# Optimization experiments

Hardware: AMD Instinct MI355X
Metric: run time of the kernel (lower is better)

The kernel has to match this reference:

```python
import jax, jax.numpy as jnp
import numpy as np

LOG0 = -1e30


def _joint_logp(enc, pred, W_enc, W_pred, b_joint, W_out, b_out):
    # enc [B,T,De], pred [B,U+1,Dp] -> log-probs over full joint lattice [B,T,U+1,V]
    ep = jnp.einsum('btd,dj->btj', enc, W_enc)          # [B,T,J]
    pp = jnp.einsum('bud,dj->buj', pred, W_pred)        # [B,U+1,J]
    h = jnp.tanh(ep[:, :, None, :] + pp[:, None, :, :] + b_joint)  # [B,T,U+1,J]
    logits = jnp.einsum('btuj,jv->btuv', h, W_out) + b_out          # [B,T,U+1,V]
    return jax.nn.log_softmax(logits, axis=-1)


def _rnnt_loss(enc, pred, W_enc, W_pred, b_joint, W_out, b_out,
               labels, enc_lens, label_lens, blank_id):
    B, T, _ = enc.shape
    Up1 = pred.shape[1]
    U = Up1 - 1
    logp = _joint_logp(enc, pred, W_enc, W_pred, b_joint, W_out, b_out)
    blank_lp = logp[..., blank_id]                       # [B,T,U+1]
    # label_lp[b,t,u] = logp[b,t,u,labels[b,u]]
    label_lp = jnp.take_along_axis(
        logp[:, :, :U, :], labels[:, None, :, None], axis=3)[..., 0]  # [B,T,U]

    # alpha recurrence over t; the inner u-recurrence
    #   a[u] = logaddexp(alpha[u]+blank_lp[u], a[u-1]+label_lp[u-1])
    # is a log-space linear recurrence solved in parallel via cumlogsumexp:
    #   with L[u] = sum_{j<u} label_lp[j],  a = L + cumlogsumexp(c - L),  c = alpha + blank_lp
    def step(alpha, t):
        blp = blank_lp[:, t]                              # [B,U+1]
        llp = label_lp[:, t]                              # [B,U]
        c = alpha + blp
        L = jnp.concatenate(
            [jnp.zeros((B, 1), dtype=alpha.dtype), jnp.cumsum(llp, axis=1)], axis=1)
        a_new = L + jax.lax.cumlogsumexp(c - L, axis=1)
        alpha = jnp.where((t < enc_lens)[:, None], a_new, alpha)
        return alpha, None

    alpha0 = jnp.full((B, Up1), LOG0, dtype=enc.dtype).at[:, 0].set(0.0)
    alpha, _ = jax.lax.scan(step, alpha0, jnp.arange(T))

    bidx = jnp.arange(B)
    terminal_blank = blank_lp[bidx, enc_lens - 1, label_lens]   # [B]
    alpha_U = alpha[bidx, label_lens]                           # [B]
    return jnp.mean(-(alpha_U + terminal_blank))


def setup_inputs() -> dict:
    key = jax.random.key(0)
    ks = jax.random.split(key, 9)
    B, T, U = 8, 256, 64
    De, Dp, J, V = 640, 640, 512, 1024
    enc = jax.random.normal(ks[0], (B, T, De), dtype=jnp.float32)
    pred = jax.random.normal(ks[1], (B, U + 1, Dp), dtype=jnp.float32)
    labels = jax.random.randint(ks[2], (B, U), 1, V).astype(jnp.int32)
    enc_lens = jax.random.randint(ks[3], (B,), T // 2, T + 1).astype(jnp.int32)
    label_lens = jax.random.randint(ks[4], (B,), U // 2, U + 1).astype(jnp.int32)
    W_enc = jax.random.normal(ks[5], (De, J), dtype=jnp.float32) * (De ** -0.5)
    W_pred = jax.random.normal(ks[6], (Dp, J), dtype=jnp.float32) * (Dp ** -0.5)
    b_joint = jnp.zeros((J,), dtype=jnp.float32)
    W_out = jax.random.normal(ks[7], (J, V), dtype=jnp.float32) * (J ** -0.5)
    b_out = jnp.zeros((V,), dtype=jnp.float32)
    return {"enc": enc, "pred": pred, "W_enc": W_enc, "W_pred": W_pred,
            "b_joint": b_joint, "W_out": W_out, "b_out": b_out,
            "labels": labels, "enc_lens": enc_lens, "label_lens": label_lens,
            "blank_id": 0}


def reference(enc, pred, W_enc, W_pred, b_joint, W_out, b_out,
              labels, enc_lens, label_lens, blank_id):
    return _rnnt_loss(enc, pred, W_enc, W_pred, b_joint, W_out, b_out,
                      labels, enc_lens, label_lens, blank_id)
```

## Files before the change

kernel.cpp:

```cpp
#include <hip/hip_runtime.h>
#include <math.h>

#define B_   8
#define T_   256
#define U_   64
#define UP1  65
#define DE   640
#define J_   512
#define V_   1024
#define NCELL (B_ * T_ * UP1)
#define LOG0 -1e30f
#define NSEG 8
#define SEGLEN 32
#define MLD  66

typedef __attribute__((ext_vector_type(4))) float f32x4;

template<int CTRL, int RM>
__device__ __forceinline__ float dppz(float x) {
    return __builtin_bit_cast(float,
        __builtin_amdgcn_update_dpp(0, __builtin_bit_cast(int, x), CTRL, RM, 0xf, false));
}
template<int CTRL, int RM>
__device__ __forceinline__ float dpps(float x) {
    int xi = __builtin_bit_cast(int, x);
    return __builtin_bit_cast(float,
        __builtin_amdgcn_update_dpp(xi, xi, CTRL, RM, 0xf, false));
}
__device__ __forceinline__ float wave_prefix_sum(float v) {
    v += dppz<0x111, 0xf>(v);
    v += dppz<0x112, 0xf>(v);
    v += dppz<0x114, 0xf>(v);
    v += dppz<0x118, 0xf>(v);
    v += dppz<0x142, 0xa>(v);
    v += dppz<0x143, 0xc>(v);
    return v;
}
__device__ __forceinline__ float wave_max_all(float v) {
    v = fmaxf(v, dpps<0x111, 0xf>(v));
    v = fmaxf(v, dpps<0x112, 0xf>(v));
    v = fmaxf(v, dpps<0x114, 0xf>(v));
    v = fmaxf(v, dpps<0x118, 0xf>(v));
    v = fmaxf(v, dpps<0x142, 0xa>(v));
    v = fmaxf(v, dpps<0x143, 0xc>(v));
    return __builtin_bit_cast(float,
        __builtin_amdgcn_readlane(__builtin_bit_cast(int, v), 63));
}
__device__ __forceinline__ float rdlane(float v, int l) {
    return __builtin_bit_cast(float,
        __builtin_amdgcn_readlane(__builtin_bit_cast(int, v), l));
}

__device__ __forceinline__ unsigned hb8(unsigned m, unsigned cb) {
    return m * 512u + (cb ^ ((m & 15u) << 3));
}

__global__ __launch_bounds__(256) void gemm_in(const float* __restrict__ A,
                                               const float* __restrict__ W,
                                               const float* __restrict__ bias,
                                               float* __restrict__ C, int M) {
    __shared__ float As[16][32];
    __shared__ float Bs[16][64];
    int tid  = threadIdx.x;
    int row0 = blockIdx.x * 32;
    int col0 = blockIdx.y * 64;
    int tx = tid & 15, ty = tid >> 4;
    float acc[2][4] = {};
    int ar  = tid >> 3;
    int ak2 = (tid & 7) * 2;
    int bkr = tid >> 4;
    int bcq = tid & 15;
    for (int k0 = 0; k0 < DE; k0 += 16) {
        float2 av = make_float2(0.f, 0.f);
        int arow = row0 + ar;
        if (arow < M) av = *(const float2*)&A[arow * DE + k0 + ak2];
        As[ak2][ar]     = av.x;
        As[ak2 + 1][ar] = av.y;
        *(float4*)&Bs[bkr][bcq * 4] = *(const float4*)&W[(k0 + bkr) * J_ + col0 + bcq * 4];
        __syncthreads();
#pragma unroll
        for (int k = 0; k < 16; ++k) {
            float a0 = As[k][ty * 2], a1 = As[k][ty * 2 + 1];
            float4 b4 = *(const float4*)&Bs[k][tx * 4];
            float b[4] = {b4.x, b4.y, b4.z, b4.w};
#pragma unroll
            for (int j = 0; j < 4; ++j) {
                acc[0][j] += a0 * b[j];
                acc[1][j] += a1 * b[j];
            }
        }
        __syncthreads();
    }
#pragma unroll
    for (int i = 0; i < 2; ++i) {
        int row = row0 + ty * 2 + i;
        if (row >= M) continue;
#pragma unroll
        for (int j = 0; j < 4; ++j) {
            int col = col0 + tx * 4 + j;
            float v = acc[i][j];
            if (bias) v += bias[col];
            C[row * J_ + col] = v;
        }
    }
}

__global__ __launch_bounds__(256) void wt_kernel(const float* __restrict__ W,
                                                 unsigned char* __restrict__ Wf) {
    __shared__ float tile[32][33];
    int tid = threadIdx.x;
    int tx = tid & 31, ty = tid >> 5;
    int v0 = blockIdx.x * 32, k0 = blockIdx.y * 32;
#pragma unroll
    for (int i = 0; i < 4; ++i)
        tile[ty + i * 8][tx] = W[(size_t)(k0 + ty + i * 8) * V_ + v0 + tx];
    __syncthreads();
    if (tid < 128) {
        int vl = tid >> 2, lg = tid & 3;
        int v  = v0 + vl;
        float x[8];
#pragma unroll
        for (int j = 0; j < 8; ++j) x[j] = tile[lg * 8 + j][vl];
        int lo = 0, hi = 0;
        lo = __builtin_amdgcn_cvt_pk_fp8_f32(x[0], x[1], lo, false);
        lo = __builtin_amdgcn_cvt_pk_fp8_f32(x[2], x[3], lo, true);
        hi = __builtin_amdgcn_cvt_pk_fp8_f32(x[4], x[5], hi, false);
        hi = __builtin_amdgcn_cvt_pk_fp8_f32(x[6], x[7], hi, true);
        int tl = v >> 4, ln = v & 15, kt = k0 >> 5;
        *(int2*)(Wf + tl * 8192 + kt * 512 + (lg * 16 + ln) * 8) = make_int2(lo, hi);
    }
}

__global__ __launch_bounds__(512) void hgen_kernel(const float* __restrict__ ep,
                                                   const float* __restrict__ pp,
                                                   unsigned char* __restrict__ hG) {
    int tid  = threadIdx.x;
    int tile = blockIdx.x;
    unsigned char* outb = hG + (size_t)tile * 32768;
#pragma unroll
    for (int i = 0; i < 4; ++i) {
        int g   = tid + i * 512;
        int row = g >> 5;
        int lin9 = (g & 31) * 16;
        unsigned swz = ((unsigned)(row & 15)) << 3;
        int k0   = lin9 ^ (int)(swz & ~8u);
        int swap = row & 1;
        int cell = tile * 64 + row;
        unsigned epRow = (unsigned)cell / 65u;
        int u = cell - (int)epRow * 65;
        int b = (int)(epRow >> 8);
        const float* epr = ep + (size_t)epRow * J_ + k0;
        const float* ppr = pp + (size_t)(b * UP1 + u) * J_ + k0;
        float t[16];
#pragma unroll
        for (int q = 0; q < 4; ++q) {
            float4 e = *(const float4*)(epr + q * 4);
            float4 p = *(const float4*)(ppr + q * 4);
            float xs[4] = {e.x + p.x, e.y + p.y, e.z + p.z, e.w + p.w};
#pragma unroll
            for (int j = 0; j < 4; ++j) {
                float e2 = __expf(2.f * xs[j]);
                t[q * 4 + j] = 1.f - 2.f / (e2 + 1.f);
            }
        }
        int a0 = 0, a1 = 0, b0 = 0, b1 = 0;
        a0 = __builtin_amdgcn_cvt_pk_fp8_f32(t[0], t[1], a0, false);
        a0 = __builtin_amdgcn_cvt_pk_fp8_f32(t[2], t[3], a0, true);
        a1 = __builtin_amdgcn_cvt_pk_fp8_f32(t[4], t[5], a1, false);
        a1 = __builtin_amdgcn_cvt_pk_fp8_f32(t[6], t[7], a1, true);
        b0 = __builtin_amdgcn_cvt_pk_fp8_f32(t[8], t[9], b0, false);
        b0 = __builtin_amdgcn_cvt_pk_fp8_f32(t[10], t[11], b0, true);
        b1 = __builtin_amdgcn_cvt_pk_fp8_f32(t[12], t[13], b1, false);
        b1 = __builtin_amdgcn_cvt_pk_fp8_f32(t[14], t[15], b1, true);
        int4 w = swap ? make_int4(b0, b1, a0, a1) : make_int4(a0, a1, b0, b1);
        *(int4*)(outb + g * 16) = w;
    }
}

__global__ __launch_bounds__(256, 3) void joint_mfma(const unsigned char* __restrict__ hG,
                                                     const unsigned char* __restrict__ Wf,
                                                     const float* __restrict__ bout,
                                                     const int* __restrict__ labels,
                                                     const int* __restrict__ pblank,
                                                     float* __restrict__ Spart,
                                                     float* __restrict__ blp,
                                                     float* __restrict__ llp) {
    __shared__ __align__(16) unsigned char hB[64 * 512];
    __shared__ float ps[4][64];

    int tid  = threadIdx.x;
    int bx   = blockIdx.x;
    int tile = (bx >> 5) * 8 + (bx & 7);
    int bh   = (bx >> 3) & 3;
    int c0   = tile * 64;
    int wc = tid >> 6, lane = tid & 63;
    int lg = lane >> 4, ln = lane & 15;

    const long* wfbL = (const long*)Wf + (((bh << 4) + (wc << 2)) << 10) + lane;

    long bf[3][4];
    long af[2][4];

    {
        int4 v[8];
        const int4* g = (const int4*)(hG + (size_t)tile * 32768) + tid;
#pragma unroll
        for (int i = 0; i < 8; ++i) v[i] = g[i * 256];
#pragma unroll
        for (int ni = 0; ni < 4; ++ni) bf[0][ni] = wfbL[ni * 1024];
#pragma unroll
        for (int ni = 0; ni < 4; ++ni) bf[1][ni] = wfbL[ni * 1024 + 64];
#pragma unroll
        for (int i = 0; i < 8; ++i) ((int4*)hB)[tid + i * 256] = v[i];
    }
    __syncthreads();

    f32x4 acc[4][4] = {};
#pragma unroll
    for (int mi = 0; mi < 4; ++mi)
        af[0][mi] = *(const long*)(hB + hb8((unsigned)(mi * 16 + ln), (unsigned)(lg * 8)));

#pragma unroll
    for (int kt = 0; kt < 16; ++kt) {
        const int cur3 = kt % 3;
        const int pf3  = (kt + 2) % 3;
        const int cur  = kt & 1, nxt = cur ^ 1;
#pragma unroll
        for (int ni = 0; ni < 4; ++ni) {
            if (kt < 14) bf[pf3][ni] = wfbL[ni * 1024 + (kt + 2) * 64];
            __builtin_amdgcn_s_setprio(1);
#pragma unroll
            for (int mi = 0; mi < 4; ++mi)
                acc[mi][ni] = __builtin_amdgcn_mfma_f32_16x16x32_fp8_fp8(
                    af[cur][mi], bf[cur3][ni], acc[mi][ni], 0, 0, 0);
            __builtin_amdgcn_s_setprio(0);
            if (ni == 1 && kt < 15) {
#pragma unroll
                for (int mi = 0; mi < 4; ++mi) {
                    unsigned m  = (unsigned)(mi * 16 + ln);
                    unsigned cb = (unsigned)((kt + 1) * 32 + lg * 8);
                    af[nxt][mi] = *(const long*)(hB + hb8(m, cb));
                }
            }
        }
    }

    float bo[4];
#pragma unroll
    for (int ni = 0; ni < 4; ++ni) bo[ni] = bout[(bh << 8) + (wc << 6) + (ni << 4) + ln];
#pragma unroll
    for (int mi = 0; mi < 4; ++mi)
#pragma unroll
        for (int ni = 0; ni < 4; ++ni)
#pragma unroll
            for (int r = 0; r < 4; ++r) acc[mi][ni][r] += bo[ni];

#pragma unroll
    for (int mi = 0; mi < 4; ++mi) {
#pragma unroll
        for (int r = 0; r < 4; ++r) {
            float s = 0.f;
#pragma unroll
            for (int ni = 0; ni < 4; ++ni) s += __expf(acc[mi][ni][r]);
            s += __shfl_xor(s, 1);
            s += __shfl_xor(s, 2);
            s += __shfl_xor(s, 4);
            s += __shfl_xor(s, 8);
            if (ln == 0) ps[wc][mi * 16 + lg * 4 + r] = s;
        }
    }
    __syncthreads();
    if (tid < 64) {
        float S = ps[0][tid] + ps[1][tid] + ps[2][tid] + ps[3][tid];
        Spart[(size_t)bh * NCELL + c0 + tid] = S;
    }

    int blank = *pblank;
#pragma unroll
    for (int mi = 0; mi < 4; ++mi) {
#pragma unroll
        for (int r = 0; r < 4; ++r) {
            int row  = mi * 16 + lg * 4 + r;
            int cell = c0 + row;
            unsigned epRow = (unsigned)cell / 65u;
            int u = cell - (int)epRow * 65;
            int b = (int)(epRow >> 8);
            int lab = (u < U_) ? labels[(b << 6) + u] : -1;
#pragma unroll
            for (int ni = 0; ni < 4; ++ni) {
                int col = (bh << 8) + (wc << 6) + (ni << 4) + ln;
                float lgt = acc[mi][ni][r];
                if (col == blank) blp[cell] = lgt;
                if (col == lab)   llp[(size_t)(((int)epRow << 6) + u)] = lgt;
            }
        }
    }
}

__global__ __launch_bounds__(256) void pass2_kernel(const float* __restrict__ Spart,
                                                    float* __restrict__ blp,
                                                    float* __restrict__ llp) {
    int idx = blockIdx.x * 256 + threadIdx.x;
    if (idx >= NCELL) return;
    float lse = __logf(Spart[idx] + Spart[NCELL + idx] +
                       Spart[2 * NCELL + idx] + Spart[3 * NCELL + idx]);
    blp[idx] -= lse;
    unsigned epRow = (unsigned)idx / 65u;
    int u = idx - (int)epRow * 65;
    if (u < U_) llp[(size_t)((epRow << 6) + u)] -= lse;
}

__global__ __launch_bounds__(64) void segscan_kernel(const float* __restrict__ blp,
                                                     const float* __restrict__ llp,
                                                     const int* __restrict__ enc_lens,
                                                     float* __restrict__ Mbuf) {
    const float K2 = 1.4426950408889634f;
    int idx  = blockIdx.x;
    int v    = idx % 65;
    int seg  = (idx / 65) % NSEG;
    int b    = idx / (65 * NSEG);
    int lane = threadIdx.x;
    int el   = enc_lens[b];
    int t0   = seg * SEGLEN;
    if (t0 >= el) return;
    const float* bb = blp + (size_t)b * T_ * UP1;
    const float* lb = llp + (size_t)b * T_ * U_;

    float bvK[SEGLEN], lvK[SEGLEN], b64K[SEGLEN];
#pragma unroll
    for (int j = 0; j < SEGLEN; ++j) {
        int t  = t0 + j;
        int tc = (t < el) ? t : (el - 1);
        bvK[j]  = bb[tc * UP1 + lane] * K2;
        b64K[j] = bb[tc * UP1 + 64] * K2;
        lvK[j]  = lb[tc * U_ + lane] * K2;
    }

    float alpha   = (lane == v) ? 0.f : LOG0;
    float alpha64 = (v == 64) ? 0.f : LOG0;

#pragma unroll
    for (int j = 0; j < SEGLEN; ++j) {
        if (t0 + j < el) {
            float P = wave_prefix_sum(lvK[j]);
            float L = dpps<0x111, 0xf>(P);
            float P15 = rdlane(P, 15), P31 = rdlane(P, 31), P47 = rdlane(P, 47);
            if (lane == 0)  L = 0.f;
            if (lane == 16) L = P15;
            if (lane == 32) L = P31;
            if (lane == 48) L = P47;
            float P63 = rdlane(P, 63);
            float x   = alpha + bvK[j] - L;
            float x64 = alpha64 + b64K[j] - P63;
            float M = fmaxf(wave_max_all(x), x64);
            float S = wave_prefix_sum(__builtin_amdgcn_exp2f(x - M));
            float S63 = rdlane(S, 63);
            alpha   = L + M + __builtin_amdgcn_logf(S);
            alpha64 = P63 + M +
                      __builtin_amdgcn_logf(S63 + __builtin_amdgcn_exp2f(x64 - M));
        }
    }

    float* col = Mbuf + ((size_t)((b * NSEG + seg) * 65 + v)) * MLD;
    col[lane] = fmaxf(alpha, LOG0);
    if (lane == 0) col[64] = fmaxf(alpha64, LOG0);
}

__global__ __launch_bounds__(64) void apply_kernel(const float* __restrict__ Mbuf,
                                                   const float* __restrict__ blp,
                                                   const int* __restrict__ enc_lens,
                                                   const int* __restrict__ label_lens,
                                                   float* __restrict__ lossBuf) {
    __shared__ float Ml[65 * MLD];
    __shared__ float xv[66];
    const float K2  = 1.4426950408889634f;
    const float LN2 = 0.6931471805599453f;
    int b    = blockIdx.x;
    int lane = threadIdx.x;
    int el = enc_lens[b];
    int ll = label_lens[b];

    xv[lane] = (lane == 0) ? 0.f : LOG0;
    if (lane == 0) xv[64] = LOG0;
    __syncthreads();

    for (int seg = 0; seg < NSEG; ++seg) {
        if (seg * SEGLEN >= el) break;
        const float* src = Mbuf + (size_t)((b * NSEG + seg) * 65) * MLD;
        for (int i = lane; i < 65 * MLD; i += 64) Ml[i] = src[i];
        __syncthreads();
        float m = LOG0;
#pragma unroll 5
        for (int vv = 0; vv < 65; ++vv) m = fmaxf(m, Ml[vv * MLD + lane] + xv[vv]);
        m = fmaxf(m, LOG0);
        float s = 0.f;
#pragma unroll 5
        for (int vv = 0; vv < 65; ++vv)
            s += __builtin_amdgcn_exp2f(Ml[vv * MLD + lane] + xv[vv] - m);
        float y = fmaxf(m + __builtin_amdgcn_logf(s), LOG0);
        float t64  = xv[lane] + Ml[lane * MLD + 64];
        float t64b = xv[64] + Ml[64 * MLD + 64];
        float m64 = fmaxf(fmaxf(wave_max_all(t64), t64b), LOG0);
        float s64 = rdlane(wave_prefix_sum(__builtin_amdgcn_exp2f(t64 - m64)), 63);
        s64 += __builtin_amdgcn_exp2f(t64b - m64);
        float y64 = fmaxf(m64 + __builtin_amdgcn_logf(s64), LOG0);
        __syncthreads();
        xv[lane] = y;
        if (lane == 0) xv[64] = y64;
        __syncthreads();
    }

    if (lane == 0) {
        float aU = (ll < 64) ? xv[ll] : xv[64];
        float term = blp[(size_t)b * T_ * UP1 + (el - 1) * UP1 + ll] * K2;
        lossBuf[b] = -(aU + term) * LN2;
    }
}

__global__ __launch_bounds__(64) void finalize_kernel(const float* __restrict__ lossBuf,
                                                      float* __restrict__ out) {
    if (threadIdx.x == 0) {
        float s = 0.f;
        for (int i = 0; i < B_; ++i) s += lossBuf[i];
        out[0] = s / (float)B_;
    }
}

extern "C" void kernel_launch(void* const* d_in, const int* in_sizes, int n_in,
                              void* d_out, int out_size, void* d_ws, size_t ws_size,
                              hipStream_t stream) {
    (void)in_sizes; (void)n_in; (void)out_size; (void)ws_size;
    const float* enc        = (const float*)d_in[0];
    const float* pred       = (const float*)d_in[1];
    const float* W_enc      = (const float*)d_in[2];
    const float* W_pred     = (const float*)d_in[3];
    const float* b_joint    = (const float*)d_in[4];
    const float* W_out      = (const float*)d_in[5];
    const float* b_out      = (const float*)d_in[6];
    const int*   labels     = (const int*)d_in[7];
    const int*   enc_lens   = (const int*)d_in[8];
    const int*   label_lens = (const int*)d_in[9];
    const int*   blank_id   = (const int*)d_in[10];

    float* ep  = (float*)d_ws;
    float* pp  = ep  + (size_t)B_ * T_ * J_;
    float* blp = pp  + (size_t)B_ * UP1 * J_;
    float* llp = blp + (size_t)B_ * T_ * UP1;
    unsigned char* Wf = (unsigned char*)(llp + (size_t)B_ * T_ * U_);
    float* Spart = (float*)(Wf + (size_t)V_ * J_);
    unsigned char* hG = (unsigned char*)(Spart + (size_t)4 * NCELL);
    float* lossBuf = (float*)(hG + (size_t)NCELL * 512);
    float* Mbuf    = lossBuf + 64;

    wt_kernel<<<dim3(V_ / 32, J_ / 32), dim3(256), 0, stream>>>(W_out, Wf);
    gemm_in<<<dim3((B_ * T_ + 31) / 32, J_ / 64), dim3(256), 0, stream>>>(
        enc, W_enc, b_joint, ep, B_ * T_);
    gemm_in<<<dim3((B_ * UP1 + 31) / 32, J_ / 64), dim3(256), 0, stream>>>(
        pred, W_pred, nullptr, pp, B_ * UP1);
    hgen_kernel<<<dim3(NCELL / 64), dim3(512), 0, stream>>>(ep, pp, hG);
    joint_mfma<<<dim3(NCELL / 64 * 4), dim3(256), 0, stream>>>(
        hG, Wf, b_out, labels, blank_id, Spart, blp, llp);
    pass2_kernel<<<dim3((NCELL + 255) / 256), dim3(256), 0, stream>>>(Spart, blp, llp);
    segscan_kernel<<<dim3(B_ * NSEG * 65), dim3(64), 0, stream>>>(blp, llp, enc_lens,
                                                                  Mbuf);
    apply_kernel<<<dim3(B_), dim3(64), 0, stream>>>(Mbuf, blp, enc_lens, label_lens,
                                                    lossBuf);
    finalize_kernel<<<dim3(1), dim3(64), 0, stream>>>(lossBuf, (float*)d_out);
}
```

Measured before the change: 314.3 us.

## Replace FP32 input projection GEMMs with bf16 MFMA GEMM and prep kernel

Replaces the two scalar FP32 shared-memory GEMMs for the encoder and predictor projections with a prep kernel and a single MFMA GEMM. The prep kernel converts enc, pred and the weights to bf16, pre-swizzling the weights into MFMA fragment layout. The GEMM uses one 64-thread wave per 64x64 tile and prefetches operands through registers. This targets the FP32 VALU cost of the projections. It adds a conversion launch and lowers the projection inputs to bf16 precision. It also reuses the hG buffer as scratch before hgen overwrites it.

```diff
diff --git a/kernel.cpp b/kernel.cpp
--- a/kernel.cpp
+++ b/kernel.cpp
@@ -15,6 +15,13 @@
 #define MLD  66
 
 typedef __attribute__((ext_vector_type(4))) float f32x4;
+typedef __attribute__((ext_vector_type(8))) short short8;
+
+__device__ __forceinline__ unsigned short f2bf(float x) {
+    union { float f; unsigned int u; } c; c.f = x;
+    unsigned int r = (c.u + 0x7fffu + ((c.u >> 16) & 1u)) >> 16;
+    return (unsigned short)r;
+}
 
 template<int CTRL, int RM>
 __device__ __forceinline__ float dppz(float x) {
@@ -55,52 +62,126 @@
     return m * 512u + (cb ^ ((m & 15u) << 3));
 }
 
-__global__ __launch_bounds__(256) void gemm_in(const float* __restrict__ A,
-                                               const float* __restrict__ W,
-                                               const float* __restrict__ bias,
-                                               float* __restrict__ C, int M) {
-    __shared__ float As[16][32];
-    __shared__ float Bs[16][64];
-    int tid  = threadIdx.x;
-    int row0 = blockIdx.x * 32;
-    int col0 = blockIdx.y * 64;
-    int tx = tid & 15, ty = tid >> 4;
-    float acc[2][4] = {};
-    int ar  = tid >> 3;
-    int ak2 = (tid & 7) * 2;
-    int bkr = tid >> 4;
-    int bcq = tid & 15;
-    for (int k0 = 0; k0 < DE; k0 += 16) {
-        float2 av = make_float2(0.f, 0.f);
-        int arow = row0 + ar;
-        if (arow < M) av = *(const float2*)&A[arow * DE + k0 + ak2];
-        As[ak2][ar]     = av.x;
-        As[ak2 + 1][ar] = av.y;
-        *(float4*)&Bs[bkr][bcq * 4] = *(const float4*)&W[(k0 + bkr) * J_ + col0 + bcq * 4];
-        __syncthreads();
-#pragma unroll
-        for (int k = 0; k < 16; ++k) {
-            float a0 = As[k][ty * 2], a1 = As[k][ty * 2 + 1];
-            float4 b4 = *(const float4*)&Bs[k][tx * 4];
-            float b[4] = {b4.x, b4.y, b4.z, b4.w};
-#pragma unroll
-            for (int j = 0; j < 4; ++j) {
-                acc[0][j] += a0 * b[j];
-                acc[1][j] += a1 * b[j];
+__global__ __launch_bounds__(256) void prep_kernel(const float* __restrict__ We,
+                                                   const float* __restrict__ Wp,
+                                                   const float* __restrict__ enc,
+                                                   const float* __restrict__ pred,
+                                                   unsigned short* __restrict__ wf2e,
+                                                   unsigned short* __restrict__ wf2p,
+                                                   unsigned short* __restrict__ encB,
+                                                   unsigned short* __restrict__ predB) {
+    int bx = blockIdx.x, tid = threadIdx.x;
+    if (bx < 320) {
+        const float* W = (bx < 160) ? We : Wp;
+        unsigned short* dst = (bx < 160) ? wf2e : wf2p;
+        int gid = ((bx < 160) ? bx : bx - 160) * 256 + tid;
+        int lane = gid & 63, ktl = gid >> 6;
+        int kt = ktl % 20, tl = ktl / 20;
+        int lg = lane >> 4, ln = lane & 15;
+        int col = tl * 16 + ln;
+        short8 v;
+#pragma unroll
+        for (int j = 0; j < 8; ++j)
+            v[j] = (short)f2bf(W[(size_t)(kt * 32 + lg * 8 + j) * J_ + col]);
+        *(short8*)(dst + (size_t)gid * 8) = v;
+    } else if (bx < 960) {
+        int gid = (bx - 320) * 256 + tid;
+        const float* s = enc + (size_t)gid * 8;
+        float4 a = *(const float4*)s, b = *(const float4*)(s + 4);
+        short8 v;
+        v[0] = (short)f2bf(a.x); v[1] = (short)f2bf(a.y);
+        v[2] = (short)f2bf(a.z); v[3] = (short)f2bf(a.w);
+        v[4] = (short)f2bf(b.x); v[5] = (short)f2bf(b.y);
+        v[6] = (short)f2bf(b.z); v[7] = (short)f2bf(b.w);
+        *(short8*)(encB + (size_t)gid * 8) = v;
+    } else {
+        int gid = (bx - 960) * 256 + tid;
+        if (gid < 41600) {
+            const float* s = pred + (size_t)gid * 8;
+            float4 a = *(const float4*)s, b = *(const float4*)(s + 4);
+            short8 v;
+            v[0] = (short)f2bf(a.x); v[1] = (short)f2bf(a.y);
+            v[2] = (short)f2bf(a.z); v[3] = (short)f2bf(a.w);
+            v[4] = (short)f2bf(b.x); v[5] = (short)f2bf(b.y);
+            v[6] = (short)f2bf(b.z); v[7] = (short)f2bf(b.w);
+            *(short8*)(predB + (size_t)gid * 8) = v;
+        }
+    }
+}
+
+__global__ __launch_bounds__(64) void gemm_mfma(const unsigned short* __restrict__ encB,
+                                                const unsigned short* __restrict__ predB,
+                                                const unsigned short* __restrict__ wf2e,
+                                                const unsigned short* __restrict__ wf2p,
+                                                const float* __restrict__ bj,
+                                                float* __restrict__ ep,
+                                                float* __restrict__ pp) {
+    int rt = blockIdx.x, ct = blockIdx.y;
+    int lane = threadIdx.x;
+    const unsigned short* A;
+    const short8* wp;
+    float* C;
+    const float* bias;
+    int M, row0;
+    if (rt < 32) { A = encB;  wp = (const short8*)wf2e; C = ep; bias = bj;      M = 2048; row0 = rt * 64; }
+    else         { A = predB; wp = (const short8*)wf2p; C = pp; bias = nullptr; M = 520;  row0 = (rt - 32) * 64; }
+    int lg = lane >> 4, ln = lane & 15;
+
+    int r_[4];
+#pragma unroll
+    for (int mi = 0; mi < 4; ++mi) {
+        int rr = row0 + mi * 16 + ln;
+        r_[mi] = (rr < M) ? rr : (M - 1);
+    }
+
+#define WIDX(NI, KT) (((size_t)((ct * 4 + (NI)) * 20 + (KT))) * 64 + lane)
+    short8 bf[3][4], af[2][4];
+#pragma unroll
+    for (int ni = 0; ni < 4; ++ni) bf[0][ni] = wp[WIDX(ni, 0)];
+#pragma unroll
+    for (int ni = 0; ni < 4; ++ni) bf[1][ni] = wp[WIDX(ni, 1)];
+#pragma unroll
+    for (int mi = 0; mi < 4; ++mi)
+        af[0][mi] = *(const short8*)(A + (size_t)r_[mi] * DE + lg * 8);
+
+    f32x4 acc[4][4] = {};
+#pragma unroll
+    for (int kt = 0; kt < 20; ++kt) {
+        const int cur3 = kt % 3;
+        const int pf3  = (kt + 2) % 3;
+        const int cur  = kt & 1, nxt = cur ^ 1;
+#pragma unroll
+        for (int ni = 0; ni < 4; ++ni) {
+            if (kt < 18) bf[pf3][ni] = wp[WIDX(ni, kt + 2)];
+            __builtin_amdgcn_s_setprio(1);
+#pragma unroll
+            for (int mi = 0; mi < 4; ++mi)
+                acc[mi][ni] = __builtin_amdgcn_mfma_f32_16x16x32_bf16(
+                    af[cur][mi], bf[cur3][ni], acc[mi][ni], 0, 0, 0);
+            __builtin_amdgcn_s_setprio(0);
+            if (ni == 1 && kt < 19) {
+#pragma unroll
+                for (int mi = 0; mi < 4; ++mi)
+                    af[nxt][mi] = *(const short8*)(A + (size_t)r_[mi] * DE +
+                                                   (kt + 1) * 32 + lg * 8);
             }
         }
-        __syncthreads();
-    }
-#pragma unroll
-    for (int i = 0; i < 2; ++i) {
-        int row = row0 + ty * 2 + i;
-        if (row >= M) continue;
-#pragma unroll
-        for (int j = 0; j < 4; ++j) {
-            int col = col0 + tx * 4 + j;
-            float v = acc[i][j];
-            if (bias) v += bias[col];
-            C[row * J_ + col] = v;
+    }
+#undef WIDX
+
+#pragma unroll
+    for (int mi = 0; mi < 4; ++mi) {
+#pragma unroll
+        for (int r = 0; r < 4; ++r) {
+            int row = row0 + mi * 16 + lg * 4 + r;
+            if (row >= M) continue;
+#pragma unroll
+            for (int ni = 0; ni < 4; ++ni) {
+                int col = ct * 64 + ni * 16 + ln;
+                float v = acc[mi][ni][r];
+                if (bias) v += bias[col];
+                C[(size_t)row * J_ + col] = v;
+            }
         }
     }
 }
@@ -452,11 +533,16 @@
     float* lossBuf = (float*)(hG + (size_t)NCELL * 512);
     float* Mbuf    = lossBuf + 64;
 
+    unsigned short* encB  = (unsigned short*)hG;
+    unsigned short* predB = encB + (size_t)2048 * DE;
+    unsigned short* wf2e  = predB + (size_t)520 * DE;
+    unsigned short* wf2p  = wf2e + (size_t)DE * J_;
+
     wt_kernel<<<dim3(V_ / 32, J_ / 32), dim3(256), 0, stream>>>(W_out, Wf);
-    gemm_in<<<dim3((B_ * T_ + 31) / 32, J_ / 64), dim3(256), 0, stream>>>(
-        enc, W_enc, b_joint, ep, B_ * T_);
-    gemm_in<<<dim3((B_ * UP1 + 31) / 32, J_ / 64), dim3(256), 0, stream>>>(
-        pred, W_pred, nullptr, pp, B_ * UP1);
+    prep_kernel<<<dim3(1123), dim3(256), 0, stream>>>(W_enc, W_pred, enc, pred,
+                                                      wf2e, wf2p, encB, predB);
+    gemm_mfma<<<dim3(41, 8), dim3(64), 0, stream>>>(encB, predB, wf2e, wf2p, b_joint,
+                                                    ep, pp);
     hgen_kernel<<<dim3(NCELL / 64), dim3(512), 0, stream>>>(ep, pp, hG);
     joint_mfma<<<dim3(NCELL / 64 * 4), dim3(256), 0, stream>>>(
         hG, Wf, b_out, labels, blank_id, Spart, blp, llp);
```

Result: faster. 268.0 us (-14.7%).
